# Performance work log

Measured on AMD Instinct MI355X. Metric: run time of the kernel, lower is better.

## Reference

```python
import jax, jax.numpy as jnp
import numpy as np

NF = 3
THRESH = 0.05
MODES1 = [0, 64, 32]
MODES2 = [0, 64, 32]
LEVEL = 3
WIDTHS = [32, 64, 64]


def _cgelu(z):
    # split-complex GELU: gelu on real and imag parts independently
    return jax.nn.gelu(z.real) + 1j * jax.nn.gelu(z.imag)


def _forward(x_real, x_imag, Re,
             p_w1_r, p_w1_i, p_b1_r, p_b1_i, p_w2_r, p_w2_i, p_b2_r, p_b2_i,
             w0_r, w0_i, wd1_r, wd1_i, wu1_r, wu1_i, wd2_r, wd2_i, wu2_r, wu2_i,
             S1, S2):
    c = lambda r, i: (r + 1j * i).astype(jnp.complex64)
    x = c(x_real, x_imag)                       # (B, C0, S1, M2) half-spectrum
    B = x.shape[0]
    M1, M2 = S1 // 2, S2 // 2 + 1
    m1_list = [M1, MODES1[1], MODES1[2]]
    m2_list = [M2, MODES2[1], MODES2[2]]

    # --- get_k: fractional powers of signed wavenumbers ---
    h1, h2 = S1 // 2, S2 // 2
    kx1 = jnp.concatenate([jnp.arange(0, S1 - h1), jnp.arange(-h1, 0)]).reshape(S1, 1)
    kx2 = jnp.concatenate([jnp.arange(0, S2 - h2), jnp.arange(-h2, 0)]).reshape(1, S2)
    k = jnp.stack([jnp.broadcast_to(kx1, (S1, S2)),
                   jnp.broadcast_to(kx2, (S1, S2))], 0)[..., :M2]   # (2, S1, M2)
    pw = (jnp.arange(1, NF + 1, dtype=jnp.float32) / NF).reshape(NF, 1, 1, 1)
    k_mat = jnp.power(k[None].astype(jnp.complex64), pw)            # (NF, 2, S1, M2)
    k_mat = jnp.broadcast_to(k_mat.reshape(1, 2 * NF, S1, M2), (B, 2 * NF, S1, M2))

    # --- embed_re: fractional powers of Reynolds number ---
    re_pw = (jnp.arange(1, NF + 1, dtype=jnp.float32) / NF).reshape(1, NF, 1, 1)
    re_mat = jnp.power(Re, re_pw).astype(jnp.complex64)             # (B, NF, 1, 1)
    re_mat = jnp.broadcast_to(re_mat, (B, NF, S1, M2))

    feat = jnp.concatenate([k_mat, re_mat], axis=1)                 # (B, 3*NF, S1, M2)

    # --- complex 1x1-conv MLP p ---
    h = jnp.einsum('bixy,oi->boxy', feat, c(p_w1_r, p_w1_i)) + c(p_b1_r, p_b1_i)[None, :, None, None]
    h = _cgelu(h)
    re_feature = jnp.einsum('bixy,oi->boxy', h, c(p_w2_r, p_w2_i)) + c(p_b2_r, p_b2_i)[None, :, None, None]

    x = x * re_feature
    x = jnp.where(jnp.abs(x) > THRESH, x, jnp.zeros((), x.dtype))   # sparsity mask

    # level 0 (skip_in is all-ones complex)
    x1 = x + 1.0
    x1 = _cgelu(jnp.einsum('bixy,io->boxy', x1, c(w0_r, w0_i)))

    Wd = [None, c(wd1_r, wd1_i), c(wd2_r, wd2_i)]
    Wu = [None, c(wu1_r, wu1_i), c(wu2_r, wu2_i)]

    xs = [x1]
    for i in range(1, LEVEL):  # down path: corner mode truncation + channel mix
        m1, m2 = m1_list[i], m2_list[i]
        x2 = jnp.concatenate([x1[:, :, :m1, :m2], x1[:, :, -m1:, :m2]], axis=2)
        x1 = _cgelu(jnp.einsum('bixy,io->boxy', x2, Wd[i])) + 1.0
        xs.append(x1)

    skip_out = list(xs)
    for i in range(LEVEL - 1, 0, -1):  # up path: channel mix + corner add
        u = _cgelu(jnp.einsum('bixy,io->boxy', xs[i], Wu[i]))
        m1, m2 = m1_list[i], m2_list[i]
        prev = xs[i - 1]
        prev = prev.at[:, :, :m1, :m2].add(u[:, :, :m1, :m2])
        prev = prev.at[:, :, -m1:, :m2].add(u[:, :, -m1:, :m2])
        xs[i - 1] = prev
        skip_out[i - 1] = prev  # torch mutates in place, so skip_out aliases

    return (xs[0], skip_out[0], skip_out[1], skip_out[2])


def setup_inputs() -> dict:
    key = jax.random.key(0)
    B, S1, S2 = 8, 256, 256
    M2 = S2 // 2 + 1
    ks = jax.random.split(key, 24)
    f = lambda k, s: jax.random.normal(k, s, jnp.float32)
    w = lambda k, s: 0.05 * jax.random.normal(k, s, jnp.float32)
    return {
        'x_real': f(ks[0], (B, 32, S1, M2)),
        'x_imag': f(ks[1], (B, 32, S1, M2)),
        'Re': jax.random.uniform(ks[2], (B, 1, 1, 1), jnp.float32, 0.5, 2.0),
        'p_w1_r': w(ks[3], (32, 9)), 'p_w1_i': w(ks[4], (32, 9)),
        'p_b1_r': w(ks[5], (32,)), 'p_b1_i': w(ks[6], (32,)),
        'p_w2_r': w(ks[7], (32, 32)), 'p_w2_i': w(ks[8], (32, 32)),
        'p_b2_r': w(ks[9], (32,)), 'p_b2_i': w(ks[10], (32,)),
        'w0_r': w(ks[11], (32, 32)), 'w0_i': w(ks[12], (32, 32)),
        'wd1_r': w(ks[13], (32, 64)), 'wd1_i': w(ks[14], (32, 64)),
        'wu1_r': w(ks[15], (64, 32)), 'wu1_i': w(ks[16], (64, 32)),
        'wd2_r': w(ks[17], (64, 64)), 'wd2_i': w(ks[18], (64, 64)),
        'wu2_r': w(ks[19], (64, 64)), 'wu2_i': w(ks[20], (64, 64)),
        'S1': S1, 'S2': S2,
    }


def reference(x_real, x_imag, Re,
              p_w1_r, p_w1_i, p_b1_r, p_b1_i, p_w2_r, p_w2_i, p_b2_r, p_b2_i,
              w0_r, w0_i, wd1_r, wd1_i, wu1_r, wu1_i, wd2_r, wd2_i, wu2_r, wu2_i,
              S1, S2):
    return _forward(x_real, x_imag, Re,
                    p_w1_r, p_w1_i, p_b1_r, p_b1_i, p_w2_r, p_w2_i, p_b2_r, p_b2_i,
                    w0_r, w0_i, wd1_r, wd1_i, wu1_r, wu1_i, wd2_r, wd2_i, wu2_r, wu2_i,
                    S1, S2)
```

## Files before the change

kernel.cpp:

```cpp
#include <hip/hip_runtime.h>

typedef long long i64;

#define BB   8
#define SS1  256
#define MM2  129
#define SP0  (SS1*MM2)

#define O0 0LL
#define O1 8454144LL
#define O2 16908288LL
#define O3 21102592LL

__device__ __forceinline__ float ldf(const float* p, i64 i, i64 cap) {
    return (i >= 0 && i < cap) ? p[i] : 0.0f;
}
__device__ __forceinline__ void stf(float* p, i64 i, i64 cap, float v) {
    if (i >= 0 && i < cap) p[i] = v;
}

__device__ __forceinline__ float tanh_fast(float x) {
    float a = fabsf(x);
    float t = __expf(-2.0f * a);
    float r = (1.0f - t) * __builtin_amdgcn_rcpf(1.0f + t);
    return copysignf(r, x);
}
__device__ __forceinline__ float gelu_f(float x) {
    float inner = 0.7978845608028654f * (x + 0.044715f * x * x * x);
    return 0.5f * x * (1.0f + tanh_fast(inner));
}

__device__ __forceinline__ void compute_features(
    int b, int x, int y, const float* __restrict__ Re,
    float* fr, float* fi, float* rp)
{
    float kv0 = (x < 128) ? (float)x : (float)(x - 256);
    float kv1 = (y < 128) ? (float)y : -128.0f;
    const float P[3] = {1.0f/3.0f, 2.0f/3.0f, 1.0f};
    #pragma unroll
    for (int d = 0; d < 2; d++) {
        float k = d ? kv1 : kv0;
        float lg = __logf(fabsf(k));
        #pragma unroll
        for (int f = 0; f < 3; f++) {
            int c = f * 2 + d;
            float m = __expf(P[f] * lg);
            if (k == 0.0f)      { fr[c] = 0.0f; fi[c] = 0.0f; }
            else if (k > 0.0f)  { fr[c] = m;    fi[c] = 0.0f; }
            else {
                float ang = P[f] * 3.14159274101257f;
                fr[c] = m * __cosf(ang);
                fi[c] = m * __sinf(ang);
            }
        }
    }
    float lre = __logf(Re[b]);
    #pragma unroll
    for (int f = 0; f < 3; f++) rp[f] = __expf(P[f] * lre);
}

__global__ __launch_bounds__(256) void k_level0(
    const float* __restrict__ xr, const float* __restrict__ xi,
    const float* __restrict__ Re,
    const float* __restrict__ w1r, const float* __restrict__ w1i,
    const float* __restrict__ b1r, const float* __restrict__ b1i,
    const float* __restrict__ w2r, const float* __restrict__ w2i,
    const float* __restrict__ b2r, const float* __restrict__ b2i,
    const float* __restrict__ w0r, const float* __restrict__ w0i,
    float* __restrict__ of, i64 capf)
{
    int idx = blockIdx.x * 256 + threadIdx.x;
    if (idx >= BB * SP0) return;
    int y  = idx % MM2;
    int t2 = idx / MM2;
    int x  = t2 % SS1;
    int b  = t2 / SS1;

    float fr[6], fi[6], rp[3];
    compute_features(b, x, y, Re, fr, fi, rp);

    float hr[32], hi[32];
    #pragma unroll
    for (int o = 0; o < 32; o++) {
        float ar = b1r[o], ai = b1i[o];
        #pragma unroll
        for (int i = 0; i < 6; i++) {
            float wr = w1r[o * 9 + i], wi = w1i[o * 9 + i];
            ar += wr * fr[i] - wi * fi[i];
            ai += wr * fi[i] + wi * fr[i];
        }
        #pragma unroll
        for (int f = 0; f < 3; f++) {
            ar += w1r[o * 9 + 6 + f] * rp[f];
            ai += w1i[o * 9 + 6 + f] * rp[f];
        }
        hr[o] = gelu_f(ar);
        hi[o] = gelu_f(ai);
    }

    float acc[32];
    #pragma unroll
    for (int o = 0; o < 32; o++) acc[o] = 0.0f;

    const float TH2 = 0.05f * 0.05f;
    i64 base0 = (i64)b * 32 * SP0 + (i64)x * MM2 + y;
    for (int c = 0; c < 32; c++) {
        float rr0 = b2r[c], ri0 = b2i[c], rr1 = 0.0f, ri1 = 0.0f;
        #pragma unroll
        for (int i = 0; i < 16; i++) {
            float wr = w2r[c * 32 + i], wi = w2i[c * 32 + i];
            rr0 += wr * hr[i] - wi * hi[i];
            ri0 += wr * hi[i] + wi * hr[i];
        }
        #pragma unroll
        for (int i = 16; i < 32; i++) {
            float wr = w2r[c * 32 + i], wi = w2i[c * 32 + i];
            rr1 += wr * hr[i] - wi * hi[i];
            ri1 += wr * hi[i] + wi * hr[i];
        }
        float rrs = rr0 + rr1, ris = ri0 + ri1;
        float xre = xr[base0 + (i64)c * SP0];
        float xim = xi[base0 + (i64)c * SP0];
        float pr = xre * rrs - xim * ris;
        float pi = xre * ris + xim * rrs;
        if (pr * pr + pi * pi <= TH2) { pr = 0.0f; pi = 0.0f; }
        float vr_c = pr + 1.0f;
        float vi_c = pi;
        #pragma unroll
        for (int o = 0; o < 32; o++) {
            float wr = w0r[c * 32 + o], wi = w0i[c * 32 + o];
            acc[o] += wr * vr_c - wi * vi_c;
        }
    }

    #pragma unroll
    for (int o = 0; o < 32; o++) {
        float g = gelu_f(acc[o]);
        i64 oi = base0 + (i64)o * SP0;
        stf(of, O0 + oi, capf, g);
        stf(of, O1 + oi, capf, g);
    }
}

#define PH  0
#define PV  32
#define PX1 64
#define PV1 96
#define PV2 160

__global__ __launch_bounds__(512, 4) void k_branch1(
    const float* __restrict__ xr, const float* __restrict__ xi,
    const float* __restrict__ Re,
    const float* __restrict__ w1r, const float* __restrict__ w1i,
    const float* __restrict__ b1r, const float* __restrict__ b1i,
    const float* __restrict__ w2r, const float* __restrict__ w2i,
    const float* __restrict__ b2r, const float* __restrict__ b2i,
    const float* __restrict__ w0r, const float* __restrict__ w0i,
    const float* __restrict__ wd1r, const float* __restrict__ wd1i,
    const float* __restrict__ wu1r, const float* __restrict__ wu1i,
    float* __restrict__ of, i64 capf)
{
    int base = blockIdx.x * 8;
    int y0 = base & 63;
    int r1 = (base >> 6) & 127;
    int b  = base >> 13;
    if ((y0 < 32) && (r1 < 32 || r1 >= 96)) return;
    int x0 = (r1 < 64) ? r1 : r1 + 128;

    __shared__ float2 s_w2t[1024];
    __shared__ float2 s_w0[1024];
    __shared__ float2 s_wd1[2048];
    __shared__ float2 s_wu1[2048];
    __shared__ float2 s_pt[8][160];
    __shared__ float  s_u[8][32];

    for (int t = threadIdx.x; t < 1024; t += 512) {
        int c = t >> 5, i = t & 31;
        s_w2t[i * 32 + c] = make_float2(w2r[t], w2i[t]);
        s_w0[t] = make_float2(w0r[t], w0i[t]);
    }
    for (int t = threadIdx.x; t < 2048; t += 512) {
        s_wd1[t] = make_float2(wd1r[t], wd1i[t]);
        s_wu1[t] = make_float2(wu1r[t], wu1i[t]);
    }

    int p = threadIdx.x >> 6;
    int lane = threadIdx.x & 63;
    int y = y0 + p;

    if (lane < 32) {
        float fr[6], fi[6], rp[3];
        compute_features(b, x0, y, Re, fr, fi, rp);
        int o = lane;
        float ar = b1r[o], ai = b1i[o];
        #pragma unroll
        for (int i = 0; i < 6; i++) {
            float wr = w1r[o * 9 + i], wi = w1i[o * 9 + i];
            ar += wr * fr[i] - wi * fi[i];
            ai += wr * fi[i] + wi * fr[i];
        }
        #pragma unroll
        for (int f = 0; f < 3; f++) {
            ar += w1r[o * 9 + 6 + f] * rp[f];
            ai += w1i[o * 9 + 6 + f] * rp[f];
        }
        s_pt[p][PH + o] = make_float2(gelu_f(ar), gelu_f(ai));
    }
    __syncthreads();

    if (lane < 32) {
        int c = lane;
        float rr = b2r[c], ri = b2i[c];
        #pragma unroll
        for (int i = 0; i < 32; i++) {
            float2 w = s_w2t[i * 32 + c];
            float2 h = s_pt[p][PH + i];
            rr += w.x * h.x - w.y * h.y;
            ri += w.x * h.y + w.y * h.x;
        }
        i64 xoff = ((i64)b * 32 + c) * SP0 + (i64)x0 * MM2 + y;
        float xre = xr[xoff], xim = xi[xoff];
        float pr = xre * rr - xim * ri;
        float pi = xre * ri + xim * rr;
        const float TH2 = 0.05f * 0.05f;
        if (pr * pr + pi * pi <= TH2) { pr = 0.0f; pi = 0.0f; }
        s_pt[p][PV + c] = make_float2(pr + 1.0f, pi);
    }
    __syncthreads();

    {
        int o = lane & 31, part = lane >> 5;
        const float* vv = (const float*)&s_pt[p][PV];
        int ia = part ? 1 : 0, ib = part ? 0 : 1;
        float sgn = part ? 1.0f : -1.0f;
        float a = 0.0f;
        #pragma unroll
        for (int c2 = 0; c2 < 32; c2++) {
            float2 w = s_w0[c2 * 32 + o];
            a += w.x * vv[2 * c2 + ia] + sgn * w.y * vv[2 * c2 + ib];
        }
        a = gelu_f(a);
        ((float*)&s_pt[p][PX1 + o])[part] = a;
    }
    __syncthreads();

    {
        float ar = 0.0f, ai = 0.0f;
        #pragma unroll
        for (int i2 = 0; i2 < 32; i2++) {
            float2 w = s_wd1[i2 * 64 + lane];
            float2 x1 = s_pt[p][PX1 + i2];
            ar += w.x * x1.x - w.y * x1.y;
            ai += w.x * x1.y + w.y * x1.x;
        }
        s_pt[p][PV1 + lane] = make_float2(gelu_f(ar) + 1.0f, gelu_f(ai));
    }
    __syncthreads();

    {
        int o = threadIdx.x >> 3, ty = threadIdx.x & 7;
        float v = s_pt[ty][PV1 + o].x;
        stf(of, O2 + ((i64)((i64)b * 64 + o) * 128 + r1) * 64 + (y0 + ty), capf, v);
    }

    {
        int o = lane & 31, half = lane >> 5;
        float acc = 0.0f;
        #pragma unroll
        for (int c2 = 0; c2 < 32; c2++) {
            int c = half * 32 + c2;
            float2 w = s_wu1[c * 32 + o];
            float2 v1 = s_pt[p][PV1 + c];
            acc += w.x * v1.x - w.y * v1.y;
        }
        acc += __shfl_xor(acc, 32);
        if (lane < 32) s_u[p][o] = gelu_f(acc);
    }
    __syncthreads();

    if (threadIdx.x < 256) {
        int o = threadIdx.x >> 3, ty = threadIdx.x & 7;
        i64 oi = ((i64)b * 32 + o) * SP0 + (i64)x0 * MM2 + (y0 + ty);
        float cur = ldf(of, O0 + oi, capf) + s_u[ty][o];
        stf(of, O0 + oi, capf, cur);
        stf(of, O1 + oi, capf, cur);
    }
}

__global__ __launch_bounds__(512, 4) void k_branch2(
    const float* __restrict__ xr, const float* __restrict__ xi,
    const float* __restrict__ Re,
    const float* __restrict__ w1r, const float* __restrict__ w1i,
    const float* __restrict__ b1r, const float* __restrict__ b1i,
    const float* __restrict__ w2r, const float* __restrict__ w2i,
    const float* __restrict__ b2r, const float* __restrict__ b2i,
    const float* __restrict__ w0r, const float* __restrict__ w0i,
    const float* __restrict__ wd1r, const float* __restrict__ wd1i,
    const float* __restrict__ wu1r, const float* __restrict__ wu1i,
    const float* __restrict__ wd2r, const float* __restrict__ wd2i,
    const float* __restrict__ wu2r, const float* __restrict__ wu2i,
    float* __restrict__ of, i64 capf)
{
    int base = blockIdx.x * 8;
    int y0 = base & 31;
    int r2 = (base >> 5) & 63;
    int b  = base >> 11;
    int r1 = (r2 < 32) ? r2 : r2 + 64;
    int x0 = (r1 < 64) ? r1 : r1 + 128;

    __shared__ float2 s_w2t[1024];
    __shared__ float2 s_w0[1024];
    __shared__ float2 s_wd1[2048];
    __shared__ float2 s_wu1[2048];
    __shared__ float2 s_pt[8][224];
    __shared__ float  s_u[8][32];

    for (int t = threadIdx.x; t < 1024; t += 512) {
        int c = t >> 5, i = t & 31;
        s_w2t[i * 32 + c] = make_float2(w2r[t], w2i[t]);
        s_w0[t] = make_float2(w0r[t], w0i[t]);
    }
    for (int t = threadIdx.x; t < 2048; t += 512) {
        s_wd1[t] = make_float2(wd1r[t], wd1i[t]);
        s_wu1[t] = make_float2(wu1r[t], wu1i[t]);
    }

    int p = threadIdx.x >> 6;
    int lane = threadIdx.x & 63;
    int y = y0 + p;

    if (lane < 32) {
        float fr[6], fi[6], rp[3];
        compute_features(b, x0, y, Re, fr, fi, rp);
        int o = lane;
        float ar = b1r[o], ai = b1i[o];
        #pragma unroll
        for (int i = 0; i < 6; i++) {
            float wr = w1r[o * 9 + i], wi = w1i[o * 9 + i];
            ar += wr * fr[i] - wi * fi[i];
            ai += wr * fi[i] + wi * fr[i];
        }
        #pragma unroll
        for (int f = 0; f < 3; f++) {
            ar += w1r[o * 9 + 6 + f] * rp[f];
            ai += w1i[o * 9 + 6 + f] * rp[f];
        }
        s_pt[p][PH + o] = make_float2(gelu_f(ar), gelu_f(ai));
    }
    __syncthreads();

    if (lane < 32) {
        int c = lane;
        float rr = b2r[c], ri = b2i[c];
        #pragma unroll
        for (int i = 0; i < 32; i++) {
            float2 w = s_w2t[i * 32 + c];
            float2 h = s_pt[p][PH + i];
            rr += w.x * h.x - w.y * h.y;
            ri += w.x * h.y + w.y * h.x;
        }
        i64 xoff = ((i64)b * 32 + c) * SP0 + (i64)x0 * MM2 + y;
        float xre = xr[xoff], xim = xi[xoff];
        float pr = xre * rr - xim * ri;
        float pi = xre * ri + xim * rr;
        const float TH2 = 0.05f * 0.05f;
        if (pr * pr + pi * pi <= TH2) { pr = 0.0f; pi = 0.0f; }
        s_pt[p][PV + c] = make_float2(pr + 1.0f, pi);
    }
    __syncthreads();

    {
        int o = lane & 31, part = lane >> 5;
        const float* vv = (const float*)&s_pt[p][PV];
        int ia = part ? 1 : 0, ib = part ? 0 : 1;
        float sgn = part ? 1.0f : -1.0f;
        float a = 0.0f;
        #pragma unroll
        for (int c2 = 0; c2 < 32; c2++) {
            float2 w = s_w0[c2 * 32 + o];
            a += w.x * vv[2 * c2 + ia] + sgn * w.y * vv[2 * c2 + ib];
        }
        a = gelu_f(a);
        ((float*)&s_pt[p][PX1 + o])[part] = a;
    }
    __syncthreads();

    {
        float ar = 0.0f, ai = 0.0f;
        #pragma unroll
        for (int i2 = 0; i2 < 32; i2++) {
            float2 w = s_wd1[i2 * 64 + lane];
            float2 x1 = s_pt[p][PX1 + i2];
            ar += w.x * x1.x - w.y * x1.y;
            ai += w.x * x1.y + w.y * x1.x;
        }
        s_pt[p][PV1 + lane] = make_float2(gelu_f(ar) + 1.0f, gelu_f(ai));
    }
    __syncthreads();

    {
        float ar = 0.0f, ai = 0.0f;
        #pragma unroll 8
        for (int c2 = 0; c2 < 64; c2++) {
            float wr = wd2r[c2 * 64 + lane], wi = wd2i[c2 * 64 + lane];
            float2 v1 = s_pt[p][PV1 + c2];
            ar += wr * v1.x - wi * v1.y;
            ai += wr * v1.y + wi * v1.x;
        }
        s_pt[p][PV2 + lane] = make_float2(gelu_f(ar) + 1.0f, gelu_f(ai));
    }
    __syncthreads();

    {
        int o = threadIdx.x >> 3, ty = threadIdx.x & 7;
        float v = s_pt[ty][PV2 + o].x;
        stf(of, O3 + ((i64)((i64)b * 64 + o) * 64 + r2) * 32 + (y0 + ty), capf, v);
    }

    {
        float ar = 0.0f, ai = 0.0f;
        #pragma unroll 8
        for (int c2 = 0; c2 < 64; c2++) {
            float wr = wu2r[c2 * 64 + lane], wi = wu2i[c2 * 64 + lane];
            float2 v2 = s_pt[p][PV2 + c2];
            ar += wr * v2.x - wi * v2.y;
            ai += wr * v2.y + wi * v2.x;
        }
        float2 v1 = s_pt[p][PV1 + lane];
        v1.x += gelu_f(ar);
        v1.y += gelu_f(ai);
        s_pt[p][PV1 + lane] = v1;
    }
    __syncthreads();

    {
        int o = threadIdx.x >> 3, ty = threadIdx.x & 7;
        float v = s_pt[ty][PV1 + o].x;
        stf(of, O2 + ((i64)((i64)b * 64 + o) * 128 + r1) * 64 + (y0 + ty), capf, v);
    }

    {
        int o = lane & 31, half = lane >> 5;
        float acc = 0.0f;
        #pragma unroll
        for (int c2 = 0; c2 < 32; c2++) {
            int c = half * 32 + c2;
            float2 w = s_wu1[c * 32 + o];
            float2 v1 = s_pt[p][PV1 + c];
            acc += w.x * v1.x - w.y * v1.y;
        }
        acc += __shfl_xor(acc, 32);
        if (lane < 32) s_u[p][o] = gelu_f(acc);
    }
    __syncthreads();

    if (threadIdx.x < 256) {
        int o = threadIdx.x >> 3, ty = threadIdx.x & 7;
        i64 oi = ((i64)b * 32 + o) * SP0 + (i64)x0 * MM2 + (y0 + ty);
        float cur = ldf(of, O0 + oi, capf) + s_u[ty][o];
        stf(of, O0 + oi, capf, cur);
        stf(of, O1 + oi, capf, cur);
    }
}

extern "C" void kernel_launch(void* const* d_in, const int* in_sizes, int n_in,
                              void* d_out, int out_size, void* d_ws, size_t ws_size,
                              hipStream_t stream) {
    const float* xr   = (const float*)d_in[0];
    const float* xi   = (const float*)d_in[1];
    const float* Re   = (const float*)d_in[2];
    const float* w1r  = (const float*)d_in[3];
    const float* w1i  = (const float*)d_in[4];
    const float* b1r  = (const float*)d_in[5];
    const float* b1i  = (const float*)d_in[6];
    const float* w2r  = (const float*)d_in[7];
    const float* w2i  = (const float*)d_in[8];
    const float* b2r  = (const float*)d_in[9];
    const float* b2i  = (const float*)d_in[10];
    const float* w0r  = (const float*)d_in[11];
    const float* w0i  = (const float*)d_in[12];
    const float* wd1r = (const float*)d_in[13];
    const float* wd1i = (const float*)d_in[14];
    const float* wu1r = (const float*)d_in[15];
    const float* wu1i = (const float*)d_in[16];
    const float* wd2r = (const float*)d_in[17];
    const float* wd2i = (const float*)d_in[18];
    const float* wu2r = (const float*)d_in[19];
    const float* wu2i = (const float*)d_in[20];

    float* of  = (float*)d_out;
    i64 capf   = (i64)out_size;

    k_level0<<<dim3((BB * SP0 + 255) / 256), 256, 0, stream>>>(
        xr, xi, Re, w1r, w1i, b1r, b1i, w2r, w2i, b2r, b2i, w0r, w0i, of, capf);
    k_branch1<<<dim3(8192), 512, 0, stream>>>(
        xr, xi, Re, w1r, w1i, b1r, b1i, w2r, w2i, b2r, b2i, w0r, w0i,
        wd1r, wd1i, wu1r, wu1i, of, capf);
    k_branch2<<<dim3(2048), 512, 0, stream>>>(
        xr, xi, Re, w1r, w1i, b1r, b1i, w2r, w2i, b2r, b2i, w0r, w0i,
        wd1r, wd1i, wu1r, wu1i, wd2r, wd2i, wu2r, wu2i, of, capf);
}
```

Baseline: 529.9 us.

## Skip branch-covered points in level0 and recompute x1 locally in branch kernels

The level-0 kernel now launches only over the spectral points that the branch kernels do not overwrite, so it no longer writes the full grid only for those values to be re-read and overwritten. The branch kernels take the level-0 value from their own recomputed shared-memory result instead of loading it back from the output. They also prefetch the input tile into shared memory with coalesced loads at kernel entry, split the first MLP across all 64 lanes, and read the wu1 weights straight from global memory to shrink shared-memory use. The correctness of the reduced index map depends on the branch kernels covering exactly the skipped region.

```diff
diff --git a/kernel.cpp b/kernel.cpp
--- a/kernel.cpp
+++ b/kernel.cpp
@@ -6,6 +6,7 @@
 #define SS1  256
 #define MM2  129
 #define SP0  (SS1*MM2)
+#define NPTS_B 24832
 
 #define O0 0LL
 #define O1 8454144LL
@@ -69,12 +70,26 @@
     const float* __restrict__ w0r, const float* __restrict__ w0i,
     float* __restrict__ of, i64 capf)
 {
+    __shared__ float4 s_w2[512];
+    for (int t = threadIdx.x; t < 512; t += 256) {
+        int e = t * 2;
+        s_w2[t] = make_float4(w2r[e], w2i[e], w2r[e + 1], w2i[e + 1]);
+    }
+    __syncthreads();
+
     int idx = blockIdx.x * 256 + threadIdx.x;
-    if (idx >= BB * SP0) return;
-    int y  = idx % MM2;
-    int t2 = idx / MM2;
-    int x  = t2 % SS1;
-    int b  = t2 / SS1;
+    if (idx >= BB * NPTS_B) return;
+    int b = idx / NPTS_B;
+    int j = idx - b * NPTS_B;
+    int x, y;
+    if (j < 16640) {
+        x = j / 65;
+        y = 64 + (j - x * 65);
+    } else {
+        int j2 = j - 16640;
+        x = 64 + (j2 >> 6);
+        y = j2 & 63;
+    }
 
     float fr[6], fi[6], rp[3];
     compute_features(b, x, y, Re, fr, fi, rp);
@@ -107,16 +122,21 @@
     for (int c = 0; c < 32; c++) {
         float rr0 = b2r[c], ri0 = b2i[c], rr1 = 0.0f, ri1 = 0.0f;
         #pragma unroll
-        for (int i = 0; i < 16; i++) {
-            float wr = w2r[c * 32 + i], wi = w2i[c * 32 + i];
-            rr0 += wr * hr[i] - wi * hi[i];
-            ri0 += wr * hi[i] + wi * hr[i];
-        }
-        #pragma unroll
-        for (int i = 16; i < 32; i++) {
-            float wr = w2r[c * 32 + i], wi = w2i[c * 32 + i];
-            rr1 += wr * hr[i] - wi * hi[i];
-            ri1 += wr * hi[i] + wi * hr[i];
+        for (int i = 0; i < 16; i += 2) {
+            float4 w = s_w2[c * 16 + (i >> 1)];
+            rr0 += w.x * hr[i]     - w.y * hi[i];
+            ri0 += w.x * hi[i]     + w.y * hr[i];
+            rr1 += w.z * hr[i + 1] - w.w * hi[i + 1];
+            ri1 += w.z * hi[i + 1] + w.w * hr[i + 1];
+        }
+        #pragma unroll
+        for (int i = 16; i < 32; i += 2) {
+            float wr0 = w2r[c * 32 + i],     wi0 = w2i[c * 32 + i];
+            float wr1 = w2r[c * 32 + i + 1], wi1 = w2i[c * 32 + i + 1];
+            rr0 += wr0 * hr[i]     - wi0 * hi[i];
+            ri0 += wr0 * hi[i]     + wi0 * hr[i];
+            rr1 += wr1 * hr[i + 1] - wi1 * hi[i + 1];
+            ri1 += wr1 * hi[i + 1] + wi1 * hr[i + 1];
         }
         float rrs = rr0 + rr1, ris = ri0 + ri1;
         float xre = xr[base0 + (i64)c * SP0];
@@ -147,6 +167,30 @@
 #define PX1 64
 #define PV1 96
 #define PV2 160
+
+#define PHASE_A()                                                             \
+    {                                                                         \
+        float fr[6], fi[6], rp[3];                                            \
+        compute_features(b, x0, y, Re, fr, fi, rp);                           \
+        int o = lane & 31, part = lane >> 5;                                  \
+        float u0[6], v0[6];                                                   \
+        _Pragma("unroll")                                                     \
+        for (int i = 0; i < 6; i++) {                                         \
+            u0[i] = part ? fi[i] : fr[i];                                     \
+            v0[i] = part ? fr[i] : -fi[i];                                    \
+        }                                                                     \
+        float a = part ? b1i[o] : b1r[o];                                     \
+        _Pragma("unroll")                                                     \
+        for (int i = 0; i < 6; i++) {                                         \
+            a += w1r[o * 9 + i] * u0[i] + w1i[o * 9 + i] * v0[i];             \
+        }                                                                     \
+        _Pragma("unroll")                                                     \
+        for (int f = 0; f < 3; f++) {                                         \
+            float w = part ? w1i[o * 9 + 6 + f] : w1r[o * 9 + 6 + f];         \
+            a += w * rp[f];                                                   \
+        }                                                                     \
+        ((float*)&s_pt[p][PH + o])[part] = gelu_f(a);                         \
+    }
 
 __global__ __launch_bounds__(512, 4) void k_branch1(
     const float* __restrict__ xr, const float* __restrict__ xi,
@@ -170,42 +214,30 @@
     __shared__ float2 s_w2t[1024];
     __shared__ float2 s_w0[1024];
     __shared__ float2 s_wd1[2048];
-    __shared__ float2 s_wu1[2048];
+    __shared__ float  s_xr[32 * 9], s_xi[32 * 9];
     __shared__ float2 s_pt[8][160];
     __shared__ float  s_u[8][32];
+
+    int tc = threadIdx.x & 255;
+    int cc = tc >> 3, ty8 = tc & 7;
+    i64 xoff = ((i64)b * 32 + cc) * SP0 + (i64)x0 * MM2 + (y0 + ty8);
+    float xreg = (threadIdx.x < 256) ? xr[xoff] : xi[xoff];
 
     for (int t = threadIdx.x; t < 1024; t += 512) {
         int c = t >> 5, i = t & 31;
         s_w2t[i * 32 + c] = make_float2(w2r[t], w2i[t]);
         s_w0[t] = make_float2(w0r[t], w0i[t]);
     }
-    for (int t = threadIdx.x; t < 2048; t += 512) {
+    for (int t = threadIdx.x; t < 2048; t += 512)
         s_wd1[t] = make_float2(wd1r[t], wd1i[t]);
-        s_wu1[t] = make_float2(wu1r[t], wu1i[t]);
-    }
 
     int p = threadIdx.x >> 6;
     int lane = threadIdx.x & 63;
     int y = y0 + p;
 
-    if (lane < 32) {
-        float fr[6], fi[6], rp[3];
-        compute_features(b, x0, y, Re, fr, fi, rp);
-        int o = lane;
-        float ar = b1r[o], ai = b1i[o];
-        #pragma unroll
-        for (int i = 0; i < 6; i++) {
-            float wr = w1r[o * 9 + i], wi = w1i[o * 9 + i];
-            ar += wr * fr[i] - wi * fi[i];
-            ai += wr * fi[i] + wi * fr[i];
-        }
-        #pragma unroll
-        for (int f = 0; f < 3; f++) {
-            ar += w1r[o * 9 + 6 + f] * rp[f];
-            ai += w1i[o * 9 + 6 + f] * rp[f];
-        }
-        s_pt[p][PH + o] = make_float2(gelu_f(ar), gelu_f(ai));
-    }
+    PHASE_A();
+    if (threadIdx.x < 256) s_xr[cc * 9 + ty8] = xreg;
+    else                   s_xi[cc * 9 + ty8] = xreg;
     __syncthreads();
 
     if (lane < 32) {
@@ -218,8 +250,7 @@
             rr += w.x * h.x - w.y * h.y;
             ri += w.x * h.y + w.y * h.x;
         }
-        i64 xoff = ((i64)b * 32 + c) * SP0 + (i64)x0 * MM2 + y;
-        float xre = xr[xoff], xim = xi[xoff];
+        float xre = s_xr[c * 9 + p], xim = s_xi[c * 9 + p];
         float pr = xre * rr - xim * ri;
         float pi = xre * ri + xim * rr;
         const float TH2 = 0.05f * 0.05f;
@@ -269,9 +300,9 @@
         #pragma unroll
         for (int c2 = 0; c2 < 32; c2++) {
             int c = half * 32 + c2;
-            float2 w = s_wu1[c * 32 + o];
+            float wr = wu1r[c * 32 + o], wi = wu1i[c * 32 + o];
             float2 v1 = s_pt[p][PV1 + c];
-            acc += w.x * v1.x - w.y * v1.y;
+            acc += wr * v1.x - wi * v1.y;
         }
         acc += __shfl_xor(acc, 32);
         if (lane < 32) s_u[p][o] = gelu_f(acc);
@@ -281,7 +312,7 @@
     if (threadIdx.x < 256) {
         int o = threadIdx.x >> 3, ty = threadIdx.x & 7;
         i64 oi = ((i64)b * 32 + o) * SP0 + (i64)x0 * MM2 + (y0 + ty);
-        float cur = ldf(of, O0 + oi, capf) + s_u[ty][o];
+        float cur = s_pt[ty][PX1 + o].x + s_u[ty][o];
         stf(of, O0 + oi, capf, cur);
         stf(of, O1 + oi, capf, cur);
     }
@@ -311,42 +342,30 @@
     __shared__ float2 s_w2t[1024];
     __shared__ float2 s_w0[1024];
     __shared__ float2 s_wd1[2048];
-    __shared__ float2 s_wu1[2048];
+    __shared__ float  s_xr[32 * 9], s_xi[32 * 9];
     __shared__ float2 s_pt[8][224];
     __shared__ float  s_u[8][32];
+
+    int tc = threadIdx.x & 255;
+    int cc = tc >> 3, ty8 = tc & 7;
+    i64 xoff = ((i64)b * 32 + cc) * SP0 + (i64)x0 * MM2 + (y0 + ty8);
+    float xreg = (threadIdx.x < 256) ? xr[xoff] : xi[xoff];
 
     for (int t = threadIdx.x; t < 1024; t += 512) {
         int c = t >> 5, i = t & 31;
         s_w2t[i * 32 + c] = make_float2(w2r[t], w2i[t]);
         s_w0[t] = make_float2(w0r[t], w0i[t]);
     }
-    for (int t = threadIdx.x; t < 2048; t += 512) {
+    for (int t = threadIdx.x; t < 2048; t += 512)
         s_wd1[t] = make_float2(wd1r[t], wd1i[t]);
-        s_wu1[t] = make_float2(wu1r[t], wu1i[t]);
-    }
 
     int p = threadIdx.x >> 6;
     int lane = threadIdx.x & 63;
     int y = y0 + p;
 
-    if (lane < 32) {
-        float fr[6], fi[6], rp[3];
-        compute_features(b, x0, y, Re, fr, fi, rp);
-        int o = lane;
-        float ar = b1r[o], ai = b1i[o];
-        #pragma unroll
-        for (int i = 0; i < 6; i++) {
-            float wr = w1r[o * 9 + i], wi = w1i[o * 9 + i];
-            ar += wr * fr[i] - wi * fi[i];
-            ai += wr * fi[i] + wi * fr[i];
-        }
-        #pragma unroll
-        for (int f = 0; f < 3; f++) {
-            ar += w1r[o * 9 + 6 + f] * rp[f];
-            ai += w1i[o * 9 + 6 + f] * rp[f];
-        }
-        s_pt[p][PH + o] = make_float2(gelu_f(ar), gelu_f(ai));
-    }
+    PHASE_A();
+    if (threadIdx.x < 256) s_xr[cc * 9 + ty8] = xreg;
+    else                   s_xi[cc * 9 + ty8] = xreg;
     __syncthreads();
 
     if (lane < 32) {
@@ -359,8 +378,7 @@
             rr += w.x * h.x - w.y * h.y;
             ri += w.x * h.y + w.y * h.x;
         }
-        i64 xoff = ((i64)b * 32 + c) * SP0 + (i64)x0 * MM2 + y;
-        float xre = xr[xoff], xim = xi[xoff];
+        float xre = s_xr[c * 9 + p], xim = s_xi[c * 9 + p];
         float pr = xre * rr - xim * ri;
         float pi = xre * ri + xim * rr;
         const float TH2 = 0.05f * 0.05f;
@@ -445,9 +463,9 @@
         #pragma unroll
         for (int c2 = 0; c2 < 32; c2++) {
             int c = half * 32 + c2;
-            float2 w = s_wu1[c * 32 + o];
+            float wr = wu1r[c * 32 + o], wi = wu1i[c * 32 + o];
             float2 v1 = s_pt[p][PV1 + c];
-            acc += w.x * v1.x - w.y * v1.y;
+            acc += wr * v1.x - wi * v1.y;
         }
         acc += __shfl_xor(acc, 32);
         if (lane < 32) s_u[p][o] = gelu_f(acc);
@@ -457,7 +475,7 @@
     if (threadIdx.x < 256) {
         int o = threadIdx.x >> 3, ty = threadIdx.x & 7;
         i64 oi = ((i64)b * 32 + o) * SP0 + (i64)x0 * MM2 + (y0 + ty);
-        float cur = ldf(of, O0 + oi, capf) + s_u[ty][o];
+        float cur = s_pt[ty][PX1 + o].x + s_u[ty][o];
         stf(of, O0 + oi, capf, cur);
         stf(of, O1 + oi, capf, cur);
     }
@@ -491,7 +509,7 @@
     float* of  = (float*)d_out;
     i64 capf   = (i64)out_size;
 
-    k_level0<<<dim3((BB * SP0 + 255) / 256), 256, 0, stream>>>(
+    k_level0<<<dim3((BB * NPTS_B + 255) / 256), 256, 0, stream>>>(
         xr, xi, Re, w1r, w1i, b1r, b1i, w2r, w2i, b2r, b2i, w0r, w0i, of, capf);
     k_branch1<<<dim3(8192), 512, 0, stream>>>(
         xr, xi, Re, w1r, w1i, b1r, b1i, w2r, w2i, b2r, b2i, w0r, w0i,
```

Measured after the change: 536.5 us. Within noise of the previous version (+1.3%).
